# Kernel tuning notes

Measured on AMD Instinct MI355X. Metric: run time of the kernel, lower is better.

The kernel has to match this reference:

```python
import jax, jax.numpy as jnp
import numpy as np

H = 16          # num heads
DH = 64         # head dim
D = H * DH      # hidden = 1024


def setup_inputs() -> dict:
    key = jax.random.key(0)
    ks = jax.random.split(key, 9)
    s = 1.0 / np.sqrt(D)
    return {
        "hidden_states": jax.random.normal(ks[0], (4, 2048, D), dtype=jnp.float32),
        "Wq": jax.random.normal(ks[1], (D, D), dtype=jnp.float32) * s,
        "bq": jax.random.normal(ks[2], (D,), dtype=jnp.float32) * 0.02,
        "Wk": jax.random.normal(ks[3], (D, D), dtype=jnp.float32) * s,
        "bk": jax.random.normal(ks[4], (D,), dtype=jnp.float32) * 0.02,
        "Wv": jax.random.normal(ks[5], (D, D), dtype=jnp.float32) * s,
        "bv": jax.random.normal(ks[6], (D,), dtype=jnp.float32) * 0.02,
        "Wo": jax.random.normal(ks[7], (D, D), dtype=jnp.float32) * s,
        "bo": jax.random.normal(ks[8], (D,), dtype=jnp.float32) * 0.02,
    }


def _split_heads(x):  # [B,S,D] -> [B,H,S,DH]
    B, S, _ = x.shape
    return x.reshape(B, S, H, DH).transpose(0, 2, 1, 3)


def reference(hidden_states, Wq, bq, Wk, bk, Wv, bv, Wo, bo):
    # torch Linear: y = x @ W.T + b  (W stored as [out, in])
    q = _split_heads(jnp.einsum('bsd,ed->bse', hidden_states, Wq) + bq)
    k = _split_heads(jnp.einsum('bsd,ed->bse', hidden_states, Wk) + bk)
    v = _split_heads(jnp.einsum('bsd,ed->bse', hidden_states, Wv) + bv)
    scores = jnp.einsum('bhqd,bhkd->bhqk', q, k) / np.sqrt(DH)
    probs = jax.nn.softmax(scores, axis=-1)  # fused softmax+matmul in original
    ctx = jnp.einsum('bhqk,bhkd->bhqd', probs, v)
    B, _, S, _ = ctx.shape
    ctx = ctx.transpose(0, 2, 1, 3).reshape(B, S, D)
    out = jnp.einsum('bsd,ed->bse', ctx, Wo) + bo
    return out  # weights are None (vis=False); dropout rate asserted 0
```

## Files before the change

kernel.cpp:

```cpp
#include <hip/hip_runtime.h>


typedef __bf16 bf16;
typedef __bf16 bf16x8 __attribute__((ext_vector_type(8)));
typedef __bf16 bf16x4 __attribute__((ext_vector_type(4)));
typedef float  floatx4 __attribute__((ext_vector_type(4)));

#define NB   4
#define SEQ  2048
#define NH   16
#define DH   64
#define DIM  1024
#define MTOT (NB * SEQ)

#define CEXP 0.18033688f

__device__ __forceinline__ floatx4 zero4() {
    floatx4 z; z[0] = 0.f; z[1] = 0.f; z[2] = 0.f; z[3] = 0.f; return z;
}

__device__ __forceinline__ void load_lds16(const bf16* g, bf16* l) {
    __builtin_amdgcn_global_load_lds(
        (__attribute__((address_space(1))) void*)g,
        (__attribute__((address_space(3))) void*)l,
        16, 0, 0);
}

__global__ __launch_bounds__(256) void cvt_all(const float* __restrict__ X,
                                               const float* __restrict__ w0,
                                               const float* __restrict__ w1,
                                               const float* __restrict__ w2,
                                               const float* __restrict__ w3,
                                               bf16* __restrict__ Xb,
                                               bf16* __restrict__ Wb) {
    const size_t MD = (size_t)MTOT * DIM;
    const size_t DD = (size_t)DIM * DIM;
    size_t i = ((size_t)blockIdx.x * 256 + threadIdx.x) * 4;
    float4 f; bf16* dst;
    if (i < MD) {
        f = *(const float4*)(X + i);
        dst = Xb + i;
    } else {
        size_t off = i - MD;
        int w = (int)(off >> 20);
        size_t wi = off & (DD - 1);
        const float* ws = (w == 0) ? w0 : (w == 1) ? w1 : (w == 2) ? w2 : w3;
        f = *(const float4*)(ws + wi);
        dst = Wb + off;
    }
    bf16x4 o;
    o[0] = (bf16)f.x; o[1] = (bf16)f.y; o[2] = (bf16)f.z; o[3] = (bf16)f.w;
    *(bf16x4*)dst = o;
}

#define QKV_TILE(T_, DO_STAGE_, WAITSTR_) do {                                 \
    const bf16* bA_ = smem + ((T_) & 3) * 16384;                               \
    const bf16* bB_ = bA_ + 8192;                                              \
    if (DO_STAGE_) {                                                           \
        bf16* sA_ = smem + (((T_) + 3) & 3) * 16384;                           \
        const int ko_ = ((T_) + 3) * 32;                                       \
        load_lds16(gA0 + ko_, sA_ + soff0);                                    \
        load_lds16(gA1 + ko_, sA_ + soff1);                                    \
        load_lds16(gB0 + ko_, sA_ + 8192 + soff0);                             \
        load_lds16(gB1 + ko_, sA_ + 8192 + soff1);                             \
    }                                                                          \
    bf16x8 afr_[4], bfg_[4];                                                   \
    _Pragma("unroll")                                                          \
    for (int mf = 0; mf < 4; mf++) afr_[mf] = *(const bf16x8*)(bA_ + aoff[mf]);\
    _Pragma("unroll")                                                          \
    for (int nf = 0; nf < 4; nf++) bfg_[nf] = *(const bf16x8*)(bB_ + boff[nf]);\
    __builtin_amdgcn_s_setprio(1);                                             \
    _Pragma("unroll")                                                          \
    for (int mf = 0; mf < 4; mf++)                                             \
        _Pragma("unroll")                                                      \
        for (int nf = 0; nf < 4; nf++)                                         \
            acc[mf][nf] = __builtin_amdgcn_mfma_f32_16x16x32_bf16(             \
                afr_[mf], bfg_[nf], acc[mf][nf], 0, 0, 0);                     \
    __builtin_amdgcn_s_setprio(0);                                             \
    _Pragma("unroll")                                                          \
    for (int mf = 0; mf < 4; mf++)                                             \
        afr_[mf] = *(const bf16x8*)(bA_ + aoff[4 + mf]);                       \
    __builtin_amdgcn_s_setprio(1);                                             \
    _Pragma("unroll")                                                          \
    for (int mf = 0; mf < 4; mf++)                                             \
        _Pragma("unroll")                                                      \
        for (int nf = 0; nf < 4; nf++)                                         \
            acc[4 + mf][nf] = __builtin_amdgcn_mfma_f32_16x16x32_bf16(         \
                afr_[mf], bfg_[nf], acc[4 + mf][nf], 0, 0, 0);                 \
    __builtin_amdgcn_s_setprio(0);                                             \
    asm volatile(WAITSTR_ ::: "memory");                                       \
    __builtin_amdgcn_s_barrier();                                              \
} while (0)

__global__ __launch_bounds__(512, 2) void gemm_qkv(const bf16* __restrict__ A,
                                                   const bf16* __restrict__ W,
                                                   const float* __restrict__ bq,
                                                   const float* __restrict__ bk,
                                                   const float* __restrict__ bv,
                                                   bf16* __restrict__ Qo,
                                                   bf16* __restrict__ Ko,
                                                   bf16* __restrict__ Vt) {
    __shared__ __align__(16) bf16 smem[4 * 16384];

    const int tid  = threadIdx.x;
    const int wave = tid >> 6, lane = tid & 63;
    const int quad = lane >> 4, l16 = lane & 15;
    const int wr = wave >> 2, wc = wave & 3;

    const int wg = (blockIdx.x & 7) * 48 + (blockIdx.x >> 3);
    const int mt = wg / 12, inner = wg % 12;
    const int sel = inner >> 2, nt = inner & 3;
    const int m0 = mt * 256, n0 = nt * 256;

    const bf16* Wsel = W + (size_t)(sel * DIM + n0) * DIM;
    const float* bias = (sel == 0) ? bq : (sel == 1) ? bk : bv;

    int aoff[8], boff[4];
#pragma unroll
    for (int mf = 0; mf < 8; mf++) {
        const int row = wr * 128 + mf * 16 + l16;
        aoff[mf] = row * 32 + ((quad ^ ((row >> 1) & 3)) * 8);
    }
#pragma unroll
    for (int nf = 0; nf < 4; nf++) {
        const int row = wc * 64 + nf * 16 + l16;
        boff[nf] = row * 32 + ((quad ^ ((row >> 1) & 3)) * 8);
    }

    const int c0 = tid, c1 = tid + 512;
    const int ra0 = c0 >> 2, qa0 = (c0 & 3) ^ ((ra0 >> 1) & 3);
    const int ra1 = c1 >> 2, qa1 = (c1 & 3) ^ ((ra1 >> 1) & 3);
    const bf16* gA0 = A + (size_t)(m0 + ra0) * DIM + qa0 * 8;
    const bf16* gA1 = A + (size_t)(m0 + ra1) * DIM + qa1 * 8;
    const bf16* gB0 = Wsel + (size_t)ra0 * DIM + qa0 * 8;
    const bf16* gB1 = Wsel + (size_t)ra1 * DIM + qa1 * 8;
    const int soff0 = (wave * 64) * 8;
    const int soff1 = (512 + wave * 64) * 8;

    floatx4 acc[8][4];
#pragma unroll
    for (int mf = 0; mf < 8; mf++)
#pragma unroll
        for (int nf = 0; nf < 4; nf++) acc[mf][nf] = zero4();

#pragma unroll
    for (int kt = 0; kt < 3; kt++) {
        bf16* sA = smem + kt * 16384;
        bf16* sB = sA + 8192;
        load_lds16(gA0 + kt * 32, sA + soff0);
        load_lds16(gA1 + kt * 32, sA + soff1);
        load_lds16(gB0 + kt * 32, sB + soff0);
        load_lds16(gB1 + kt * 32, sB + soff1);
    }
    asm volatile("s_waitcnt vmcnt(8)" ::: "memory");
    __builtin_amdgcn_s_barrier();

    const int NT = DIM / 32;
#pragma unroll 1
    for (int t = 0; t < NT - 3; t++)
        QKV_TILE(t, true, "s_waitcnt vmcnt(8)");
    QKV_TILE(NT - 3, false, "s_waitcnt vmcnt(4)");
    QKV_TILE(NT - 2, false, "s_waitcnt vmcnt(0)");
    QKV_TILE(NT - 1, false, "s_waitcnt vmcnt(0)");

    if (sel < 2) {
        bf16* C = (sel == 0) ? Qo : Ko;
        const float scale = (sel == 0) ? CEXP : 1.0f;
#pragma unroll
        for (int mf = 0; mf < 8; mf++) {
            const int rbase = m0 + wr * 128 + mf * 16 + quad * 4;
#pragma unroll
            for (int nf = 0; nf < 4; nf++) {
                const int col = n0 + wc * 64 + nf * 16 + l16;
                const float bval = bias[col];
#pragma unroll
                for (int i = 0; i < 4; i++)
                    C[(size_t)(rbase + i) * DIM + col] =
                        (bf16)((acc[mf][nf][i] + bval) * scale);
            }
        }
    } else {
        const int b  = m0 >> 11;
        const int s0 = m0 & (SEQ - 1);
#pragma unroll
        for (int mf = 0; mf < 8; mf++) {
            const int mb = wr * 128 + mf * 16 + quad * 4;
#pragma unroll
            for (int nf = 0; nf < 4; nf++) {
                const int n_loc = wc * 64 + nf * 16 + l16;
                const float bval = bias[n0 + n_loc];
                bf16x4 pk;
#pragma unroll
                for (int i = 0; i < 4; i++) pk[i] = (bf16)(acc[mf][nf][i] + bval);
                const int e = n_loc * 256 + (((mb * 2) ^ ((n_loc & 7) << 4)) >> 1);
                *(bf16x4*)(smem + e) = pk;
            }
        }
        asm volatile("s_waitcnt lgkmcnt(0)" ::: "memory");
        __builtin_amdgcn_s_barrier();
#pragma unroll
        for (int p = 0; p < 16; p++) {
            const int c = p * 512 + tid;
            const int n_loc = c >> 5, mc = (c & 31) * 8;
            const int e = n_loc * 256 + (((mc * 2) ^ ((n_loc & 7) << 4)) >> 1);
            bf16x8 v = *(const bf16x8*)(smem + e);
            const int dg = n0 + n_loc;
            const int hh = dg >> 6, d = dg & 63;
            bf16* op = Vt + ((size_t)(b * NH + hh) * DH + d) * SEQ + s0 + mc;
            *(bf16x8*)op = v;
        }
    }
}

__global__ __launch_bounds__(256) void gemm_out(const bf16* __restrict__ A,
                                                const bf16* __restrict__ W,
                                                const float* __restrict__ bias,
                                                float* __restrict__ C) {
    __shared__ __align__(16) bf16 As[128 * 32];
    __shared__ __align__(16) bf16 Bs[128 * 32];

    const int tid  = threadIdx.x;
    const int wave = tid >> 6, lane = tid & 63;
    const int quad = lane >> 4, l16 = lane & 15;
    const int m0 = blockIdx.y * 128, n0 = blockIdx.x * 128;
    const int wm = (wave & 1) * 64, wn = (wave >> 1) * 64;

    floatx4 acc[4][4];
#pragma unroll
    for (int mi = 0; mi < 4; mi++)
#pragma unroll
        for (int ni = 0; ni < 4; ni++) acc[mi][ni] = zero4();

    for (int k0 = 0; k0 < DIM; k0 += 32) {
        __syncthreads();
#pragma unroll
        for (int i = 0; i < 2; i++) {
            const int cb = wave * 128 + i * 64;
            const int c  = cb + lane;
            const int row = c >> 2;
            const int kc  = (c & 3) * 8;
            load_lds16(A + (size_t)(m0 + row) * DIM + k0 + kc, &As[cb * 8]);
            load_lds16(W + (size_t)(n0 + row) * DIM + k0 + kc, &Bs[cb * 8]);
        }
        __syncthreads();

        bf16x8 af[4], bfr[4];
#pragma unroll
        for (int mi = 0; mi < 4; mi++)
            af[mi] = *(const bf16x8*)&As[(wm + mi * 16 + l16) * 32 + quad * 8];
#pragma unroll
        for (int ni = 0; ni < 4; ni++)
            bfr[ni] = *(const bf16x8*)&Bs[(wn + ni * 16 + l16) * 32 + quad * 8];
#pragma unroll
        for (int mi = 0; mi < 4; mi++)
#pragma unroll
            for (int ni = 0; ni < 4; ni++)
                acc[mi][ni] = __builtin_amdgcn_mfma_f32_16x16x32_bf16(
                    af[mi], bfr[ni], acc[mi][ni], 0, 0, 0);
    }

#pragma unroll
    for (int mi = 0; mi < 4; mi++) {
        const int rbase = m0 + wm + mi * 16 + quad * 4;
#pragma unroll
        for (int ni = 0; ni < 4; ni++) {
            const int col = n0 + wn + ni * 16 + l16;
            const float bval = bias[col];
#pragma unroll
            for (int i = 0; i < 4; i++)
                C[(size_t)(rbase + i) * DIM + col] = acc[mi][ni][i] + bval;
        }
    }
}

#define ATTN_MFMA(A_, B_, C_) __builtin_amdgcn_mfma_f32_16x16x32_bf16(A_, B_, C_, 0, 0, 0)

#define ATTN_TILE(T_, DO_STAGE_, DO_WAIT_, WAITSTR_) do {                      \
    const int cur_ = (T_) & 3;                                                 \
    if (DO_STAGE_) {                                                           \
        const int nb_ = ((T_) + 3) & 3;                                        \
        const size_t kvn_ = (size_t)((T_) + 3) * 64;                           \
        load_lds16(kga + kvn_ * DIM, &Ks[nb_][ldsa]);                          \
        load_lds16(kgb + kvn_ * DIM, &Ks[nb_][ldsb]);                          \
        load_lds16(vga + kvn_, &Vs[nb_][ldsa]);                                \
        load_lds16(vgb + kvn_, &Vs[nb_][ldsb]);                                \
    }                                                                          \
                                                      \
    bf16x8 ke0_ = *(const bf16x8*)&Ks[cur_][koa[0]];                           \
    bf16x8 ke1_ = *(const bf16x8*)&Ks[cur_][kob[0]];                           \
    bf16x8 ko0_ = *(const bf16x8*)&Ks[cur_][koa[1]];                           \
    bf16x8 ko1_ = *(const bf16x8*)&Ks[cur_][kob[1]];                           \
    floatx4 sa0_[4], sb0_[4];                                                  \
    _Pragma("unroll")                                                          \
    for (int m = 0; m < 4; m++) {                                              \
        floatx4 sa = zero4(), sb = zero4();                                    \
        sa = ATTN_MFMA(ke0_, aq[m][0], sa);                                    \
        sa = ATTN_MFMA(ke1_, aq[m][1], sa);                                    \
        sb = ATTN_MFMA(ko0_, aq[m][0], sb);                                    \
        sb = ATTN_MFMA(ko1_, aq[m][1], sb);                                    \
        sa0_[m] = sa; sb0_[m] = sb;                                            \
    }                                                                          \
        \
    bf16x8 kf1_[4];                                                            \
    kf1_[0] = *(const bf16x8*)&Ks[cur_][koa[2]];                               \
    kf1_[1] = *(const bf16x8*)&Ks[cur_][kob[2]];                               \
    kf1_[2] = *(const bf16x8*)&Ks[cur_][koa[3]];                               \
    kf1_[3] = *(const bf16x8*)&Ks[cur_][kob[3]];                               \
    bf16x8 vf0_[4];                                                            \
    _Pragma("unroll")                                                          \
    for (int dt = 0; dt < 4; dt++)                                             \
        vf0_[dt] = *(const bf16x8*)&Vs[cur_][vo[0][dt]];                       \
               \
    bf16x8 pw0_[4];                                                            \
    _Pragma("unroll")                                                          \
    for (int m = 0; m < 4; m++) {                                              \
        bf16x8 p;                                                              \
        _Pragma("unroll")                                                      \
        for (int i = 0; i < 4; i++) {                                          \
            p[i]     = (bf16)__builtin_amdgcn_exp2f(sa0_[m][i]);               \
            p[4 + i] = (bf16)__builtin_amdgcn_exp2f(sb0_[m][i]);               \
        }                                                                      \
        pw0_[m] = p;                                                           \
    }                                                                          \
                                                                   \
    floatx4 sa1_[4], sb1_[4];                                                  \
    _Pragma("unroll")                                                          \
    for (int m = 0; m < 4; m++) {                                              \
        floatx4 sa = zero4(), sb = zero4();                                    \
        sa = ATTN_MFMA(kf1_[0], aq[m][0], sa);                                 \
        sa = ATTN_MFMA(kf1_[1], aq[m][1], sa);                                 \
        sb = ATTN_MFMA(kf1_[2], aq[m][0], sb);                                 \
        sb = ATTN_MFMA(kf1_[3], aq[m][1], sb);                                 \
        sa1_[m] = sa; sb1_[m] = sb;                                            \
    }                                                                          \
                   \
    bf16x8 vf1_[4];                                                            \
    _Pragma("unroll")                                                          \
    for (int dt = 0; dt < 4; dt++)                                             \
        vf1_[dt] = *(const bf16x8*)&Vs[cur_][vo[1][dt]];                       \
    bf16x8 pw1_[4];                                                            \
    _Pragma("unroll")                                                          \
    for (int m = 0; m < 4; m++) {                                              \
        _Pragma("unroll")                                                      \
        for (int dt = 0; dt < 4; dt++)                                         \
            acc[m][dt] = ATTN_MFMA(pw0_[m], vf0_[dt], acc[m][dt]);             \
        accl[m] = ATTN_MFMA(pw0_[m], ones8, accl[m]);                          \
        bf16x8 p;                                                              \
        _Pragma("unroll")                                                      \
        for (int i = 0; i < 4; i++) {                                          \
            p[i]     = (bf16)__builtin_amdgcn_exp2f(sa1_[m][i]);               \
            p[4 + i] = (bf16)__builtin_amdgcn_exp2f(sb1_[m][i]);               \
        }                                                                      \
        pw1_[m] = p;                                                           \
    }                                                                          \
                                                                   \
    _Pragma("unroll")                                                          \
    for (int m = 0; m < 4; m++) {                                              \
        _Pragma("unroll")                                                      \
        for (int dt = 0; dt < 4; dt++)                                         \
            acc[m][dt] = ATTN_MFMA(pw1_[m], vf1_[dt], acc[m][dt]);             \
        accl[m] = ATTN_MFMA(pw1_[m], ones8, accl[m]);                          \
    }                                                                          \
    if (DO_WAIT_) asm volatile(WAITSTR_ ::: "memory");                         \
    __builtin_amdgcn_s_barrier();                                              \
} while (0)

__global__ __launch_bounds__(256, 2) void attn_kernel(const bf16* __restrict__ Q,
                                                      const bf16* __restrict__ K,
                                                      const bf16* __restrict__ Vt,
                                                      bf16* __restrict__ Ctx) {
    __shared__ __align__(16) bf16 Ks[4][64 * 64];
    __shared__ __align__(16) bf16 Vs[4][64 * 64];

    const int tid  = threadIdx.x;
    const int wave = tid >> 6, lane = tid & 63;
    const int quad = lane >> 4, l16 = lane & 15;
    const int xcd = blockIdx.x & 7;
    const int j   = blockIdx.x >> 3;
    const int bh  = xcd * 8 + (j >> 3);
    const int qb  = j & 7;
    const int b   = bh >> 4, h = bh & 15;

    const size_t base_bh = (size_t)b * SEQ * DIM + (size_t)h * DH;
    const size_t base_v  = (size_t)bh * DH * SEQ;
    const int qt = qb * 256 + wave * 64;

    bf16x8 aq[4][2];
#pragma unroll
    for (int m = 0; m < 4; m++) {
        const bf16* qp = Q + base_bh + (size_t)(qt + m * 16 + l16) * DIM + quad * 8;
        aq[m][0] = *(const bf16x8*)qp;
        aq[m][1] = *(const bf16x8*)(qp + 32);
    }

    const int sc = wave * 128 + lane;
    int srow[2], scol[2];
    srow[0] = sc >> 3;        srow[1] = (sc + 64) >> 3;
    scol[0] = (sc & 7) ^ (srow[0] & 7);
    scol[1] = ((sc + 64) & 7) ^ (srow[1] & 7);
    auto kvloc = [](int r) {
        const int w = r >> 5, rw = r & 31, r4 = rw & 15;
        return w * 32 + ((rw >> 4) << 2) + ((r4 >> 2) << 3) + (r4 & 3);
    };
    const bf16* kga = K + base_bh + (size_t)kvloc(srow[0]) * DIM + scol[0] * 8;
    const bf16* kgb = K + base_bh + (size_t)kvloc(srow[1]) * DIM + scol[1] * 8;
    const bf16* vga = Vt + base_v + (size_t)srow[0] * SEQ + scol[0] * 8;
    const bf16* vgb = Vt + base_v + (size_t)srow[1] * SEQ + scol[1] * 8;
    const int ldsa = (wave * 128) * 8, ldsb = (wave * 128 + 64) * 8;

    int koa[4], kob[4], vo[2][4];
#pragma unroll
    for (int g = 0; g < 4; g++) {
        const int krow = g * 16 + l16;
        koa[g] = (krow * 8 + (quad ^ (krow & 7))) * 8;
        kob[g] = (krow * 8 + ((4 + quad) ^ (krow & 7))) * 8;
    }
#pragma unroll
    for (int w = 0; w < 2; w++)
#pragma unroll
        for (int dt = 0; dt < 4; dt++) {
            const int d = dt * 16 + l16;
            vo[w][dt] = d * 64 + ((4 * w + quad) ^ (d & 7)) * 8;
        }

    bf16x8 ones8;
#pragma unroll
    for (int i = 0; i < 8; i++) ones8[i] = (bf16)1.0f;

    floatx4 acc[4][4], accl[4];
#pragma unroll
    for (int m = 0; m < 4; m++) {
        accl[m] = zero4();
#pragma unroll
        for (int dt = 0; dt < 4; dt++) acc[m][dt] = zero4();
    }

#pragma unroll
    for (int kt = 0; kt < 3; kt++) {
        const size_t kvn = (size_t)kt * 64;
        load_lds16(kga + kvn * DIM, &Ks[kt][ldsa]);
        load_lds16(kgb + kvn * DIM, &Ks[kt][ldsb]);
        load_lds16(vga + kvn, &Vs[kt][ldsa]);
        load_lds16(vgb + kvn, &Vs[kt][ldsb]);
    }
    asm volatile("s_waitcnt vmcnt(8)" ::: "memory");
    __builtin_amdgcn_s_barrier();

    const int NT = SEQ / 64;
#pragma unroll 1
    for (int t = 0; t < NT - 3; t++)
        ATTN_TILE(t, true, true, "s_waitcnt vmcnt(8)");
    ATTN_TILE(NT - 3, false, true, "s_waitcnt vmcnt(4)");
    ATTN_TILE(NT - 2, false, true, "s_waitcnt vmcnt(0)");
    ATTN_TILE(NT - 1, false, false, "");

#pragma unroll
    for (int m = 0; m < 4; m++) {
        float inv[4];
#pragma unroll
        for (int i = 0; i < 4; i++) inv[i] = 1.0f / accl[m][i];
        bf16* cp = Ctx + base_bh + (size_t)(qt + m * 16 + quad * 4) * DIM + l16;
#pragma unroll
        for (int i = 0; i < 4; i++)
#pragma unroll
            for (int dt = 0; dt < 4; dt++)
                cp[(size_t)i * DIM + dt * 16] = (bf16)(acc[m][dt][i] * inv[i]);
    }
}

extern "C" void kernel_launch(void* const* d_in, const int* in_sizes, int n_in,
                              void* d_out, int out_size, void* d_ws, size_t ws_size,
                              hipStream_t stream) {
    const float* X  = (const float*)d_in[0];
    const float* Wq = (const float*)d_in[1];
    const float* bq = (const float*)d_in[2];
    const float* Wk = (const float*)d_in[3];
    const float* bk = (const float*)d_in[4];
    const float* Wv = (const float*)d_in[5];
    const float* bv = (const float*)d_in[6];
    const float* Wo = (const float*)d_in[7];
    const float* bo = (const float*)d_in[8];
    float* out = (float*)d_out;

    const size_t MD = (size_t)MTOT * DIM;
    const size_t DD = (size_t)DIM * DIM;

    bf16* Xb  = (bf16*)d_ws;
    bf16* Qb  = Xb + MD;
    bf16* Kb  = Qb + MD;
    bf16* Vtb = Kb + MD;
    bf16* Wqb = Vtb + MD;
    bf16* Wob = Wqb + 3 * DD;
    if (ws_size < (MD * 4 + DD * 4) * sizeof(bf16)) return;

    cvt_all<<<(int)((MD + 4 * DD) / 4 / 256), 256, 0, stream>>>(
        X, Wq, Wk, Wv, Wo, Xb, Wqb);

    gemm_qkv<<<384, 512, 0, stream>>>(Xb, Wqb, bq, bk, bv, Qb, Kb, Vtb);

    attn_kernel<<<NB * NH * (SEQ / 256), 256, 0, stream>>>(Qb, Kb, Vtb, Xb);

    gemm_out<<<dim3(8, MTOT / 128), 256, 0, stream>>>(Xb, Wob, bo, out);
}
```

Baseline: 257.6 us.

## Rewrite output projection GEMM with 4-stage LDS pipeline, swizzle, larger tiles

Replaces the simple double-synced output GEMM with a 256x128 tile kernel that prefetches three K-steps ahead into a 4-deep LDS ring using direct global-to-LDS loads and vmcnt-based waits with one barrier per step. LDS rows are XOR-swizzled to avoid bank conflicts, MFMA sections are given raised wave priority, and the 1D grid is remapped for L2 locality. It aims to hide global load latency and cut barrier overhead. The larger per-wave accumulator (8x4 fragments) raises register pressure, and the 256 blocks may underfill the CUs.

New measurement: 257.2 us (median of 2 runs). No clear change (-0.2%).

```diff
diff --git a/kernel.cpp b/kernel.cpp
--- a/kernel.cpp
+++ b/kernel.cpp
@@ -212,63 +212,125 @@
     }
 }
 
-__global__ __launch_bounds__(256) void gemm_out(const bf16* __restrict__ A,
-                                                const bf16* __restrict__ W,
-                                                const float* __restrict__ bias,
-                                                float* __restrict__ C) {
-    __shared__ __align__(16) bf16 As[128 * 32];
-    __shared__ __align__(16) bf16 Bs[128 * 32];
+#define OUT_TILE(T_, DO_STAGE_, WAITSTR_) do {                                 \
+    const bf16* bA_ = smem + ((T_) & 3) * 12288;                               \
+    const bf16* bB_ = bA_ + 8192;                                              \
+    if (DO_STAGE_) {                                                           \
+        bf16* sA_ = smem + (((T_) + 3) & 3) * 12288;                           \
+        const int ko_ = ((T_) + 3) * 32;                                       \
+        load_lds16(gA0 + ko_, sA_ + soffA0);                                   \
+        load_lds16(gA1 + ko_, sA_ + soffA1);                                   \
+        load_lds16(gA2 + ko_, sA_ + soffA2);                                   \
+        load_lds16(gA3 + ko_, sA_ + soffA3);                                   \
+        load_lds16(gB0 + ko_, sA_ + 8192 + soffB0);                            \
+        load_lds16(gB1 + ko_, sA_ + 8192 + soffB1);                            \
+    }                                                                          \
+    bf16x8 afr_[8], bfg_[4];                                                   \
+    _Pragma("unroll")                                                          \
+    for (int mf = 0; mf < 8; mf++) afr_[mf] = *(const bf16x8*)(bA_ + aoff[mf]);\
+    _Pragma("unroll")                                                          \
+    for (int nf = 0; nf < 4; nf++) bfg_[nf] = *(const bf16x8*)(bB_ + boff[nf]);\
+    __builtin_amdgcn_s_setprio(1);                                             \
+    _Pragma("unroll")                                                          \
+    for (int mf = 0; mf < 8; mf++)                                             \
+        _Pragma("unroll")                                                      \
+        for (int nf = 0; nf < 4; nf++)                                         \
+            acc[mf][nf] = __builtin_amdgcn_mfma_f32_16x16x32_bf16(             \
+                afr_[mf], bfg_[nf], acc[mf][nf], 0, 0, 0);                     \
+    __builtin_amdgcn_s_setprio(0);                                             \
+    asm volatile(WAITSTR_ ::: "memory");                                       \
+    __builtin_amdgcn_s_barrier();                                              \
+} while (0)
+
+__global__ __launch_bounds__(256, 2) void gemm_out(const bf16* __restrict__ A,
+                                                   const bf16* __restrict__ W,
+                                                   const float* __restrict__ bias,
+                                                   float* __restrict__ C) {
+    __shared__ __align__(16) bf16 smem[4 * 12288];
 
     const int tid  = threadIdx.x;
     const int wave = tid >> 6, lane = tid & 63;
     const int quad = lane >> 4, l16 = lane & 15;
-    const int m0 = blockIdx.y * 128, n0 = blockIdx.x * 128;
-    const int wm = (wave & 1) * 64, wn = (wave >> 1) * 64;
-
-    floatx4 acc[4][4];
-#pragma unroll
-    for (int mi = 0; mi < 4; mi++)
-#pragma unroll
-        for (int ni = 0; ni < 4; ni++) acc[mi][ni] = zero4();
-
-    for (int k0 = 0; k0 < DIM; k0 += 32) {
-        __syncthreads();
-#pragma unroll
-        for (int i = 0; i < 2; i++) {
-            const int cb = wave * 128 + i * 64;
-            const int c  = cb + lane;
-            const int row = c >> 2;
-            const int kc  = (c & 3) * 8;
-            load_lds16(A + (size_t)(m0 + row) * DIM + k0 + kc, &As[cb * 8]);
-            load_lds16(W + (size_t)(n0 + row) * DIM + k0 + kc, &Bs[cb * 8]);
-        }
-        __syncthreads();
-
-        bf16x8 af[4], bfr[4];
-#pragma unroll
-        for (int mi = 0; mi < 4; mi++)
-            af[mi] = *(const bf16x8*)&As[(wm + mi * 16 + l16) * 32 + quad * 8];
-#pragma unroll
-        for (int ni = 0; ni < 4; ni++)
-            bfr[ni] = *(const bf16x8*)&Bs[(wn + ni * 16 + l16) * 32 + quad * 8];
-#pragma unroll
-        for (int mi = 0; mi < 4; mi++)
-#pragma unroll
-            for (int ni = 0; ni < 4; ni++)
-                acc[mi][ni] = __builtin_amdgcn_mfma_f32_16x16x32_bf16(
-                    af[mi], bfr[ni], acc[mi][ni], 0, 0, 0);
-    }
-
-#pragma unroll
-    for (int mi = 0; mi < 4; mi++) {
-        const int rbase = m0 + wm + mi * 16 + quad * 4;
-#pragma unroll
-        for (int ni = 0; ni < 4; ni++) {
-            const int col = n0 + wn + ni * 16 + l16;
+    const int wr = wave >> 1, wc = wave & 1;
+
+    const int wg = (blockIdx.x & 7) * 32 + (blockIdx.x >> 3);
+    const int mt = wg >> 3, nt = wg & 7;
+    const int m0 = mt * 256, n0 = nt * 128;
+
+    int aoff[8], boff[4];
+#pragma unroll
+    for (int mf = 0; mf < 8; mf++) {
+        const int row = wr * 128 + mf * 16 + l16;
+        aoff[mf] = row * 32 + ((quad ^ ((row >> 1) & 3)) * 8);
+    }
+#pragma unroll
+    for (int nf = 0; nf < 4; nf++) {
+        const int row = wc * 64 + nf * 16 + l16;
+        boff[nf] = row * 32 + ((quad ^ ((row >> 1) & 3)) * 8);
+    }
+
+    int arow[4], aks[4];
+#pragma unroll
+    for (int j = 0; j < 4; j++) {
+        const int c = j * 256 + tid;
+        arow[j] = c >> 2; aks[j] = (c & 3) ^ ((arow[j] >> 1) & 3);
+    }
+    int brow[2], bks[2];
+#pragma unroll
+    for (int j = 0; j < 2; j++) {
+        const int c = j * 256 + tid;
+        brow[j] = c >> 2; bks[j] = (c & 3) ^ ((brow[j] >> 1) & 3);
+    }
+    const bf16* gA0 = A + (size_t)(m0 + arow[0]) * DIM + aks[0] * 8;
+    const bf16* gA1 = A + (size_t)(m0 + arow[1]) * DIM + aks[1] * 8;
+    const bf16* gA2 = A + (size_t)(m0 + arow[2]) * DIM + aks[2] * 8;
+    const bf16* gA3 = A + (size_t)(m0 + arow[3]) * DIM + aks[3] * 8;
+    const bf16* gB0 = W + (size_t)(n0 + brow[0]) * DIM + bks[0] * 8;
+    const bf16* gB1 = W + (size_t)(n0 + brow[1]) * DIM + bks[1] * 8;
+    const int soffA0 = (0 * 256 + wave * 64) * 8;
+    const int soffA1 = (1 * 256 + wave * 64) * 8;
+    const int soffA2 = (2 * 256 + wave * 64) * 8;
+    const int soffA3 = (3 * 256 + wave * 64) * 8;
+    const int soffB0 = (0 * 256 + wave * 64) * 8;
+    const int soffB1 = (1 * 256 + wave * 64) * 8;
+
+    floatx4 acc[8][4];
+#pragma unroll
+    for (int mf = 0; mf < 8; mf++)
+#pragma unroll
+        for (int nf = 0; nf < 4; nf++) acc[mf][nf] = zero4();
+
+#pragma unroll
+    for (int kt = 0; kt < 3; kt++) {
+        bf16* sA = smem + kt * 12288;
+        load_lds16(gA0 + kt * 32, sA + soffA0);
+        load_lds16(gA1 + kt * 32, sA + soffA1);
+        load_lds16(gA2 + kt * 32, sA + soffA2);
+        load_lds16(gA3 + kt * 32, sA + soffA3);
+        load_lds16(gB0 + kt * 32, sA + 8192 + soffB0);
+        load_lds16(gB1 + kt * 32, sA + 8192 + soffB1);
+    }
+    asm volatile("s_waitcnt vmcnt(12)" ::: "memory");
+    __builtin_amdgcn_s_barrier();
+
+    const int NT = DIM / 32;
+#pragma unroll 1
+    for (int t = 0; t < NT - 3; t++)
+        OUT_TILE(t, true, "s_waitcnt vmcnt(12)");
+    OUT_TILE(NT - 3, false, "s_waitcnt vmcnt(6)");
+    OUT_TILE(NT - 2, false, "s_waitcnt vmcnt(0)");
+    OUT_TILE(NT - 1, false, "s_waitcnt vmcnt(0)");
+
+#pragma unroll
+    for (int mf = 0; mf < 8; mf++) {
+        const int rbase = m0 + wr * 128 + mf * 16 + quad * 4;
+#pragma unroll
+        for (int nf = 0; nf < 4; nf++) {
+            const int col = n0 + wc * 64 + nf * 16 + l16;
             const float bval = bias[col];
 #pragma unroll
             for (int i = 0; i < 4; i++)
-                C[(size_t)(rbase + i) * DIM + col] = acc[mi][ni][i] + bval;
+                C[(size_t)(rbase + i) * DIM + col] = acc[mf][nf][i] + bval;
         }
     }
 }
@@ -310,7 +372,7 @@
     _Pragma("unroll")                                                          \
     for (int dt = 0; dt < 4; dt++)                                             \
         vf0_[dt] = *(const bf16x8*)&Vs[cur_][vo[0][dt]];                       \
-               \
+                                                    \
     bf16x8 pw0_[4];                                                            \
     _Pragma("unroll")                                                          \
     for (int m = 0; m < 4; m++) {                                              \
@@ -333,7 +395,7 @@
         sb = ATTN_MFMA(kf1_[3], aq[m][1], sb);                                 \
         sa1_[m] = sa; sb1_[m] = sb;                                            \
     }                                                                          \
-                   \
+                                             \
     bf16x8 vf1_[4];                                                            \
     _Pragma("unroll")                                                          \
     for (int dt = 0; dt < 4; dt++)                                             \
@@ -500,5 +562,5 @@
 
     attn_kernel<<<NB * NH * (SEQ / 256), 256, 0, stream>>>(Qb, Kb, Vtb, Xb);
 
-    gemm_out<<<dim3(8, MTOT / 128), 256, 0, stream>>>(Xb, Wob, bo, out);
-}
+    gemm_out<<<256, 256, 0, stream>>>(Xb, Wob, bo, out);
+}
```
